# Kernel optimization log

Hardware: AMD Instinct MI355X
Metric: run time of the kernel (lower is better)

## Reference

```python
import jax, jax.numpy as jnp
import numpy as np

B, C, H, W = 8, 512, 64, 64
CH = C // 2          # channels per branch after chunk
R = CH // 4          # reduced channels (reduction=4)


def conv1x1(x, w, b):
    # x: [B,c,H,W], w: [o,c], b: [o]  (1x1 conv == per-pixel matmul)
    return jnp.einsum('oc,bchw->bohw', w, x) + b[None, :, None, None]


def spatial_self_corr(x, w1, b1, w2, b2, wo, bo):
    # DANet-style position attention. x: [B,CH,H,W]
    b_, c_, h_, w_ = x.shape
    n = h_ * w_
    q = conv1x1(x, w1, b1).reshape(b_, -1, n)   # [B,R,N]
    k = conv1x1(x, w2, b2).reshape(b_, -1, n)   # [B,R,N]
    attn = jax.nn.softmax(jnp.einsum('brn,brm->bnm', q, k), axis=-1)  # [B,N,N]
    out = jnp.einsum('brn,bnm->brm', k, attn)   # v = k (reduced channels), [B,R,N]
    out = out.reshape(b_, -1, h_, w_)
    return conv1x1(out, wo, bo)                 # [B,CH,H,W]


def channel_self_corr(x, wq, bq, wk, bk, wo, bo):
    # DANet-style channel attention over reduced channels. x: [B,CH,H,W]
    b_, c_, h_, w_ = x.shape
    n = h_ * w_
    q = conv1x1(x, wq, bq).reshape(b_, -1, n)   # [B,R,N]
    k = conv1x1(x, wk, bk).reshape(b_, -1, n)   # [B,R,N]
    attn = jax.nn.softmax(jnp.einsum('brn,bsn->brs', q, k), axis=-1)  # [B,R,R]
    out = jnp.einsum('brs,bsn->brn', attn, k)   # v = k (reduced channels)
    out = out.reshape(b_, -1, h_, w_)
    return conv1x1(out, wo, bo)                 # [B,CH,H,W]


def ckam_forward(top_feat, bottom_feat, wt, bt, wb, bb,
                 s_w1, s_b1, s_w2, s_b2, s_wo, s_bo,
                 c_wq, c_bq, c_wk, c_bk, c_wo, c_bo, f_w, f_b):
    top = conv1x1(top_feat, wt, bt)
    bottom = conv1x1(bottom_feat, wb, bb)
    x = top + bottom                            # [B,C,H,W]
    x1, x2 = jnp.split(x, 2, axis=1)            # each [B,C/2,H,W]
    ssc_out = spatial_self_corr(x1, s_w1, s_b1, s_w2, s_b2, s_wo, s_bo)
    csc_out = channel_self_corr(x2, c_wq, c_bq, c_wk, c_bk, c_wo, c_bo)
    out = jnp.concatenate([ssc_out, csc_out], axis=1)  # [B,C,H,W]
    return conv1x1(out, f_w, f_b)


def setup_inputs() -> dict:
    key = jax.random.key(0)
    ks = jax.random.split(key, 24)
    s = 0.02
    d = {
        'top_feat': jax.random.normal(ks[0], (B, C, H, W), jnp.float32),
        'bottom_feat': jax.random.normal(ks[1], (B, C, H, W), jnp.float32),
        'wt': jax.random.normal(ks[2], (C, C), jnp.float32) * s,
        'bt': jnp.zeros((C,), jnp.float32),
        'wb': jax.random.normal(ks[3], (C, C), jnp.float32) * s,
        'bb': jnp.zeros((C,), jnp.float32),
        's_w1': jax.random.normal(ks[4], (R, CH), jnp.float32) * s,
        's_b1': jnp.zeros((R,), jnp.float32),
        's_w2': jax.random.normal(ks[5], (R, CH), jnp.float32) * s,
        's_b2': jnp.zeros((R,), jnp.float32),
        's_wo': jax.random.normal(ks[6], (CH, R), jnp.float32) * s,
        's_bo': jnp.zeros((CH,), jnp.float32),
        'c_wq': jax.random.normal(ks[7], (R, CH), jnp.float32) * s,
        'c_bq': jnp.zeros((R,), jnp.float32),
        'c_wk': jax.random.normal(ks[8], (R, CH), jnp.float32) * s,
        'c_bk': jnp.zeros((R,), jnp.float32),
        'c_wo': jax.random.normal(ks[9], (CH, R), jnp.float32) * s,
        'c_bo': jnp.zeros((CH,), jnp.float32),
        'f_w': jax.random.normal(ks[10], (C, C), jnp.float32) * s,
        'f_b': jnp.zeros((C,), jnp.float32),
    }
    return d


def reference(top_feat, bottom_feat, wt, bt, wb, bb,
              s_w1, s_b1, s_w2, s_b2, s_wo, s_bo,
              c_wq, c_bq, c_wk, c_bk, c_wo, c_bo, f_w, f_b):
    return ckam_forward(top_feat, bottom_feat, wt, bt, wb, bb,
                        s_w1, s_b1, s_w2, s_b2, s_wo, s_bo,
                        c_wq, c_bq, c_wk, c_bk, c_wo, c_bo, f_w, f_b)
```

## Files before the change

### kernel.cpp

```cpp
#include <hip/hip_runtime.h>

typedef unsigned short u16;
typedef unsigned int   u32;
typedef __attribute__((ext_vector_type(8))) short short8;
typedef __attribute__((ext_vector_type(4))) float f32x4;

__device__ __forceinline__ u16 f2bf(float f) {
  u32 u = __float_as_uint(f);
  u32 r = u + 0x7fffu + ((u >> 16) & 1u);
  return (u16)(r >> 16);
}

__device__ __forceinline__ void gl_lds16(const u16* g, u16* l) {
  __builtin_amdgcn_global_load_lds(
      (const __attribute__((address_space(1))) u32*)g,
      (__attribute__((address_space(3))) u32*)l, 16, 0, 0);
}

__global__ __launch_bounds__(256) void k_combine_qk(
    const float* __restrict__ wt, const float* __restrict__ bt,
    const float* __restrict__ wb, const float* __restrict__ bb,
    const float* __restrict__ s_w1, const float* __restrict__ s_b1,
    const float* __restrict__ s_w2, const float* __restrict__ s_b2,
    const float* __restrict__ c_wq, const float* __restrict__ c_bq,
    const float* __restrict__ c_wk, const float* __restrict__ c_bk,
    u16* __restrict__ Wqkb, float* __restrict__ bqk) {
  int j = blockIdx.x;
  int g = j >> 6, r = j & 63;
  const float* sw; const float* sb;
  if (g == 0)      { sw = s_w1; sb = s_b1; }
  else if (g == 1) { sw = s_w2; sb = s_b2; }
  else if (g == 2) { sw = c_wq; sb = c_bq; }
  else             { sw = c_wk; sb = c_bk; }
  int cbase = (g < 2) ? 0 : 256;

  __shared__ float swr[256];
  __shared__ float red[256];
  int t = threadIdx.x;
  swr[t] = sw[r * 256 + t];
  __syncthreads();

  float a0 = 0.f, a1 = 0.f, a2 = 0.f, a3 = 0.f;
#pragma unroll 4
  for (int c = 0; c < 256; ++c) {
    float a = swr[c];
    int row = (cbase + c) * 512;
    a0 += a * wt[row + t];
    a1 += a * wt[row + 256 + t];
    a2 += a * wb[row + t];
    a3 += a * wb[row + 256 + t];
  }
  Wqkb[j * 1024 + t]       = f2bf(a0);
  Wqkb[j * 1024 + 256 + t] = f2bf(a1);
  Wqkb[j * 1024 + 512 + t] = f2bf(a2);
  Wqkb[j * 1024 + 768 + t] = f2bf(a3);

  red[t] = swr[t] * (bt[cbase + t] + bb[cbase + t]);
  __syncthreads();
  for (int s = 128; s > 0; s >>= 1) {
    if (t < s) red[t] += red[t + s];
    __syncthreads();
  }
  if (t == 0) bqk[j] = red[0] + sb[r];
}

__global__ __launch_bounds__(128) void k_combine_f(
    const float* __restrict__ f_w, const float* __restrict__ f_b,
    const float* __restrict__ s_wo, const float* __restrict__ s_bo,
    const float* __restrict__ c_wo, const float* __restrict__ c_bo,
    u16* __restrict__ Wfb, float* __restrict__ bfb) {
  int o = blockIdx.x;
  int t = threadIdx.x;
  __shared__ float fwr[512];
  __shared__ float red[128];
  for (int i = t; i < 512; i += 128) fwr[i] = f_w[o * 512 + i];
  __syncthreads();

  float acc = 0.f;
  if (t < 64) {
#pragma unroll 4
    for (int c = 0; c < 256; ++c) acc += fwr[c] * s_wo[c * 64 + t];
  } else {
    int rr = t - 64;
#pragma unroll 4
    for (int c = 0; c < 256; ++c) acc += fwr[256 + c] * c_wo[c * 64 + rr];
  }
  Wfb[o * 128 + t] = f2bf(acc);

  red[t] = fwr[t] * s_bo[t] + fwr[t + 128] * s_bo[t + 128]
         + fwr[256 + t] * c_bo[t] + fwr[384 + t] * c_bo[t + 128];
  __syncthreads();
  for (int s = 64; s > 0; s >>= 1) {
    if (t < s) red[t] += red[t + s];
    __syncthreads();
  }
  if (t == 0) bfb[o] = red[0] + f_b[o];
}

__global__ __launch_bounds__(256) void k_gemm_qk_mfma(
    const float* __restrict__ top, const float* __restrict__ bot,
    const u16* __restrict__ Wqkb, const float* __restrict__ bqk,
    float* __restrict__ qk) {
  int b = blockIdx.z, j0 = blockIdx.y * 128, n0 = blockIdx.x * 128;
  __shared__ __align__(16) u16 Aj[2][128][32];
  __shared__ __align__(16) u16 Xs[2][128][32];
  int t = threadIdx.x;
  int wv = t >> 6, lane = t & 63;
  int wr = wv >> 1, wc = wv & 1;
  int q = lane >> 4, l = lane & 15;

  f32x4 acc[4][4];
#pragma unroll
  for (int tr = 0; tr < 4; ++tr)
#pragma unroll
    for (int tc = 0; tc < 4; ++tc) acc[tr][tc] = (f32x4){0.f, 0.f, 0.f, 0.f};

  int xn = t & 31;
  int xs = t >> 5;
  int asrow = (lane >> 2);
  int asc = (lane & 3) ^ ((lane >> 2) & 3);
  int fsw = (q ^ (l & 3)) << 4;

  float xv[16];

  auto stageA = [&](int kc, u16* dst) {
#pragma unroll
    for (int p = 0; p < 2; ++p) {
      int cI = wv * 2 + p;
      int row = cI * 16 + asrow;
      gl_lds16(Wqkb + (size_t)(j0 + row) * 1024 + kc + asc * 8, dst + cI * 512);
    }
  };
  auto loadX = [&](int kc) {
    const float* src = (kc < 512) ? top : bot;
    int c0 = kc & 511;
    const float* xb = src + (size_t)(b * 512 + c0) * 4096 + n0;
#pragma unroll
    for (int p = 0; p < 8; ++p) {
      int n = xn + 32 * (p >> 1);
      int kp = xs + 8 * (p & 1);
      xv[2 * p]     = xb[(size_t)(2 * kp) * 4096 + n];
      xv[2 * p + 1] = xb[(size_t)(2 * kp + 1) * 4096 + n];
    }
  };
  auto writeX = [&](u16* dst) {
    char* base = reinterpret_cast<char*>(dst);
#pragma unroll
    for (int p = 0; p < 8; ++p) {
      int n = xn + 32 * (p >> 1);
      int kp = xs + 8 * (p & 1);
      u32 v = (u32)f2bf(xv[2 * p]) | ((u32)f2bf(xv[2 * p + 1]) << 16);
      *reinterpret_cast<u32*>(
          base + n * 64 + ((((kp >> 2) ^ (n & 3)) << 4) | ((kp & 3) << 2))) = v;
    }
  };

  stageA(0, &Aj[0][0][0]);
  loadX(0);
  writeX(&Xs[0][0][0]);
  __syncthreads();

  int cur = 0;
  for (int it = 0; it < 32; ++it) {
    if (it + 1 < 32) {
      stageA((it + 1) * 32, &Aj[cur ^ 1][0][0]);
      loadX((it + 1) * 32);
    }
    const char* Ab = reinterpret_cast<const char*>(&Aj[cur][0][0]);
    const char* Xb = reinterpret_cast<const char*>(&Xs[cur][0][0]);
    short8 af[4], bfr[4];
#pragma unroll
    for (int tr = 0; tr < 4; ++tr) {
      int row = wr * 64 + tr * 16 + l;
      af[tr] = *reinterpret_cast<const short8*>(Ab + row * 64 + fsw);
    }
#pragma unroll
    for (int tc = 0; tc < 4; ++tc) {
      int row = wc * 64 + tc * 16 + l;
      bfr[tc] = *reinterpret_cast<const short8*>(Xb + row * 64 + fsw);
    }
#pragma unroll
    for (int tr = 0; tr < 4; ++tr)
#pragma unroll
      for (int tc = 0; tc < 4; ++tc)
        acc[tr][tc] = __builtin_amdgcn_mfma_f32_16x16x32_bf16(
            af[tr], bfr[tc], acc[tr][tc], 0, 0, 0);
    if (it + 1 < 32) writeX(&Xs[cur ^ 1][0][0]);
    __syncthreads();
    cur ^= 1;
  }

#pragma unroll
  for (int tr = 0; tr < 4; ++tr) {
    int j = j0 + wr * 64 + tr * 16 + q * 4;
    float4 bias = *reinterpret_cast<const float4*>(&bqk[j]);
#pragma unroll
    for (int tc = 0; tc < 4; ++tc) {
      int n = n0 + wc * 64 + tc * 16 + l;
      float* dst = qk + (size_t)(b * 256 + j) * 4096 + n;
      dst[0]        = acc[tr][tc][0] + bias.x;
      dst[4096]     = acc[tr][tc][1] + bias.y;
      dst[2 * 4096] = acc[tr][tc][2] + bias.z;
      dst[3 * 4096] = acc[tr][tc][3] + bias.w;
    }
  }
}

__global__ __launch_bounds__(256) void k_transpose_qk(
    const float* __restrict__ qk, u16* __restrict__ q1t, u16* __restrict__ k1t) {
  int b = blockIdx.y, n0 = blockIdx.x * 64;
  __shared__ u16 T[128][68];
  int t = threadIdx.x;
  for (int i = t; i < 8192; i += 256) {
    int j = i >> 6, n = i & 63;
    T[j][n] = f2bf(qk[((size_t)(b * 256) + j) * 4096 + n0 + n]);
  }
  __syncthreads();
  int n = t & 63, h = t >> 6;
  u16 buf[32];
#pragma unroll
  for (int jj = 0; jj < 32; ++jj) buf[jj] = T[h * 32 + jj][n];
  u16* dst;
  if (h < 2) dst = q1t + ((size_t)(b * 4096) + n0 + n) * 64 + h * 32;
  else       dst = k1t + ((size_t)(b * 4096) + n0 + n) * 64 + (h - 2) * 32;
  u32* d32 = reinterpret_cast<u32*>(dst);
#pragma unroll
  for (int k = 0; k < 16; ++k)
    d32[k] = (u32)buf[2 * k] | ((u32)buf[2 * k + 1] << 16);
}

__global__ __launch_bounds__(256) void k_sp_stats_mfma(
    const u16* __restrict__ q1t, const u16* __restrict__ k1t,
    float* __restrict__ dinv) {
  int b = blockIdx.y, n0 = blockIdx.x * 64;
  __shared__ u16 Qs[64][72];
  __shared__ float red[4][64][16];
  int t = threadIdx.x;
  int wv = t >> 6, lane = t & 63;
  int q = lane >> 4, l = lane & 15;

  {
    const u32* src = reinterpret_cast<const u32*>(q1t + ((size_t)(b * 4096) + n0) * 64);
    for (int i = t; i < 2048; i += 256) {
      int n = i >> 5, c = i & 31;
      reinterpret_cast<u32*>(&Qs[n][0])[c] = src[n * 32 + c];
    }
  }
  __syncthreads();

  short8 afr[4][2];
#pragma unroll
  for (int tn = 0; tn < 4; ++tn)
#pragma unroll
    for (int kh = 0; kh < 2; ++kh)
      afr[tn][kh] = *reinterpret_cast<const short8*>(&Qs[tn * 16 + l][kh * 32 + q * 8]);

  const u16* kbase = k1t + (size_t)b * 4096 * 64;
  float dsum[4][4];
#pragma unroll
  for (int tn = 0; tn < 4; ++tn)
#pragma unroll
    for (int i = 0; i < 4; ++i) dsum[tn][i] = 0.f;

  for (int mt = wv; mt < 64; mt += 4) {
    int m0 = mt * 64;
#pragma unroll
    for (int tm = 0; tm < 4; ++tm) {
      const u16* kp = kbase + ((size_t)(m0 + tm * 16 + l)) * 64;
      short8 b0 = *reinterpret_cast<const short8*>(kp + q * 8);
      short8 b1 = *reinterpret_cast<const short8*>(kp + 32 + q * 8);
#pragma unroll
      for (int tn = 0; tn < 4; ++tn) {
        f32x4 acc = {0.f, 0.f, 0.f, 0.f};
        acc = __builtin_amdgcn_mfma_f32_16x16x32_bf16(afr[tn][0], b0, acc, 0, 0, 0);
        acc = __builtin_amdgcn_mfma_f32_16x16x32_bf16(afr[tn][1], b1, acc, 0, 0, 0);
#pragma unroll
        for (int i = 0; i < 4; ++i) dsum[tn][i] += __expf(acc[i]);
      }
    }
  }

#pragma unroll
  for (int tn = 0; tn < 4; ++tn)
#pragma unroll
    for (int i = 0; i < 4; ++i)
      red[wv][tn * 16 + q * 4 + i][l] = dsum[tn][i];
  __syncthreads();
  if (t < 64) {
    float s = 0.f;
#pragma unroll
    for (int v = 0; v < 4; ++v)
#pragma unroll
      for (int u = 0; u < 16; ++u) s += red[v][t][u];
    dinv[(size_t)b * 4096 + n0 + t] = 1.0f / s;
  }
}

__global__ __launch_bounds__(256) void k_scale_k1d(
    const float* __restrict__ qk, const float* __restrict__ dinv,
    u16* __restrict__ k1d) {
  int b = blockIdx.x >> 6, r = blockIdx.x & 63;
  const float* src = qk + ((size_t)(b * 256) + 64 + r) * 4096;
  const float* dv = dinv + (size_t)b * 4096;
  u16* dst = k1d + ((size_t)(b * 64) + r) * 4096;
  for (int i = threadIdx.x; i < 4096; i += 256)
    dst[i] = f2bf(src[i] * dv[i]);
}

#define NSPLIT 2

__device__ __forceinline__ void stage_qk(const u16* qb, const u16* kb, int noff,
                                         u16* qdst, u16* kdst,
                                         int wv, int rsub, int scol) {
#pragma unroll
  for (int pp = 0; pp < 2; ++pp) {
    int p = wv * 2 + pp;
    int row = p * 8 + rsub;
    gl_lds16(qb + ((size_t)(noff + row)) * 64 + scol * 8, qdst + p * 512);
    gl_lds16(kb + (size_t)row * 4096 + noff + scol * 8, kdst + p * 512);
  }
}

__global__ __launch_bounds__(256) void k_sp_apply_mfma(
    const u16* __restrict__ q1t, const u16* __restrict__ k1t,
    const u16* __restrict__ k1d, float* __restrict__ spre) {
  int b = blockIdx.z, m0 = blockIdx.x * 64;
  int n_base = blockIdx.y * (4096 / NSPLIT);
  const int NT = 64 / NSPLIT;

  __shared__ __align__(16) u16 Qs[2][64][64];
  __shared__ __align__(16) u16 Ks[2][64][64];
  __shared__ __align__(16) u16 Wt[64][64];

  int t = threadIdx.x;
  int wv = t >> 6, lane = t & 63;
  int q = lane >> 4, l = lane & 15;
  int sw = l & 7;
  int rsub = lane >> 3;
  int scol = (lane & 7) ^ rsub;

  const u16* ktp = k1t + ((size_t)(b * 4096) + m0 + wv * 16 + l) * 64;
  short8 bS0 = *reinterpret_cast<const short8*>(ktp + q * 8);
  short8 bS1 = *reinterpret_cast<const short8*>(ktp + 32 + q * 8);

  const u16* qb = q1t + (size_t)b * 4096 * 64;
  const u16* kb = k1d + (size_t)b * 64 * 4096;

  f32x4 accO[4];
#pragma unroll
  for (int tr = 0; tr < 4; ++tr) accO[tr] = (f32x4){0.f, 0.f, 0.f, 0.f};

  stage_qk(qb, kb, n_base, &Qs[0][0][0], &Ks[0][0][0], wv, rsub, scol);
  __syncthreads();

  int wrow = wv * 16 + l;
  char* wp = reinterpret_cast<char*>(&Wt[wrow][0]);
  int c_a0 = (q ^ sw) << 4;
  int c_a1 = c_a0 ^ 64;

  int cur = 0;
  for (int nt = 0; nt < NT; ++nt) {
    if (nt + 1 < NT)
      stage_qk(qb, kb, n_base + (nt + 1) * 64,
               &Qs[cur ^ 1][0][0], &Ks[cur ^ 1][0][0], wv, rsub, scol);

    const u16(*Qc)[64] = Qs[cur];
    const u16(*Kc)[64] = Ks[cur];

#pragma unroll
    for (int tn = 0; tn < 4; ++tn) {
      const char* qrow = reinterpret_cast<const char*>(&Qc[tn * 16 + l][0]);
      short8 a0 = *reinterpret_cast<const short8*>(qrow + c_a0);
      short8 a1 = *reinterpret_cast<const short8*>(qrow + c_a1);
      f32x4 s = {0.f, 0.f, 0.f, 0.f};
      s = __builtin_amdgcn_mfma_f32_16x16x32_bf16(a0, bS0, s, 0, 0, 0);
      s = __builtin_amdgcn_mfma_f32_16x16x32_bf16(a1, bS1, s, 0, 0, 0);
      u16 w0 = f2bf(__expf(s[0]));
      u16 w1 = f2bf(__expf(s[1]));
      u16 w2 = f2bf(__expf(s[2]));
      u16 w3 = f2bf(__expf(s[3]));
      uint2 pk;
      pk.x = (u32)w0 | ((u32)w1 << 16);
      pk.y = (u32)w2 | ((u32)w3 << 16);
      *reinterpret_cast<uint2*>(
          wp + ((((tn * 2 + (q >> 1)) ^ sw) << 4) | ((q & 1) << 3))) = pk;
    }

    short8 bW0 = *reinterpret_cast<const short8*>(wp + c_a0);
    short8 bW1 = *reinterpret_cast<const short8*>(wp + c_a1);
#pragma unroll
    for (int tr = 0; tr < 4; ++tr) {
      const char* krow = reinterpret_cast<const char*>(&Kc[tr * 16 + l][0]);
      short8 a0 = *reinterpret_cast<const short8*>(krow + c_a0);
      short8 a1 = *reinterpret_cast<const short8*>(krow + c_a1);
      accO[tr] = __builtin_amdgcn_mfma_f32_16x16x32_bf16(a0, bW0, accO[tr], 0, 0, 0);
      accO[tr] = __builtin_amdgcn_mfma_f32_16x16x32_bf16(a1, bW1, accO[tr], 0, 0, 0);
    }

    __syncthreads();
    cur ^= 1;
  }

#pragma unroll
  for (int tr = 0; tr < 4; ++tr)
#pragma unroll
    for (int i = 0; i < 4; ++i)
      atomicAdd(&spre[(size_t)(b * 64 + tr * 16 + q * 4 + i) * 4096 + m0 + wrow],
                accO[tr][i]);
}

__global__ __launch_bounds__(256) void k_ch_scores(
    const float* __restrict__ qk, float* __restrict__ part) {
  int b = blockIdx.y, ch = blockIdx.x;
  const float* q2 = qk + (size_t)(b * 256 + 128) * 4096;
  const float* k2 = qk + (size_t)(b * 256 + 192) * 4096;
  __shared__ float Qs[64][65];
  __shared__ float Ks[64][65];
  int t = threadIdx.x, ti = t >> 4, tj = t & 15;
  float acc[4][4] = {};

  for (int sub = 0; sub < 2; ++sub) {
    int n0 = ch * 128 + sub * 64;
    __syncthreads();
    for (int i = t; i < 4096; i += 256) {
      int r = i >> 6, n = i & 63;
      Qs[r][n] = q2[(size_t)r * 4096 + n0 + n];
      Ks[r][n] = k2[(size_t)r * 4096 + n0 + n];
    }
    __syncthreads();
#pragma unroll
    for (int n = 0; n < 64; ++n) {
      float qa[4], ka[4];
#pragma unroll
      for (int i = 0; i < 4; ++i) qa[i] = Qs[ti * 4 + i][n];
#pragma unroll
      for (int jx = 0; jx < 4; ++jx) ka[jx] = Ks[tj * 4 + jx][n];
#pragma unroll
      for (int i = 0; i < 4; ++i)
#pragma unroll
        for (int jx = 0; jx < 4; ++jx) acc[i][jx] += qa[i] * ka[jx];
    }
  }
#pragma unroll
  for (int i = 0; i < 4; ++i)
#pragma unroll
    for (int jx = 0; jx < 4; ++jx)
      part[(size_t)(b * 32 + ch) * 4096 + (ti * 4 + i) * 64 + tj * 4 + jx] = acc[i][jx];
}

__global__ __launch_bounds__(64) void k_ch_softmax(
    const float* __restrict__ part, float* __restrict__ attn2) {
  int bid = blockIdx.x;
  int b = bid >> 6, r = bid & 63;
  int s = threadIdx.x;
  const float* p0 = part + (size_t)(b * 32) * 4096 + r * 64 + s;
  float sum = 0.f;
#pragma unroll
  for (int c = 0; c < 32; ++c) sum += p0[(size_t)c * 4096];
  float mx = sum;
#pragma unroll
  for (int o = 32; o > 0; o >>= 1) mx = fmaxf(mx, __shfl_xor(mx, o));
  float e = __expf(sum - mx);
  float den = e;
#pragma unroll
  for (int o = 32; o > 0; o >>= 1) den += __shfl_xor(den, o);
  attn2[(size_t)b * 4096 + r * 64 + s] = e / den;
}

__global__ __launch_bounds__(256) void k_ch_apply(
    const float* __restrict__ qk, const float* __restrict__ attn2,
    float* __restrict__ cpre) {
  int b = blockIdx.y;
  int t = threadIdx.x;
  int n = blockIdx.x * 64 + (t & 63);
  int qr = t >> 6;
  const float* k2 = qk + (size_t)(b * 256 + 192) * 4096;
  __shared__ float As[64][64];
  {
    float4* As4 = reinterpret_cast<float4*>(&As[0][0]);
    const float4* a4 = reinterpret_cast<const float4*>(attn2 + (size_t)b * 4096);
    for (int i = t; i < 1024; i += 256) As4[i] = a4[i];
  }
  __syncthreads();

  float acc[16];
#pragma unroll
  for (int rr = 0; rr < 16; ++rr) acc[rr] = 0.f;
  for (int s4 = 0; s4 < 64; s4 += 4) {
    float kv0 = k2[(size_t)(s4 + 0) * 4096 + n];
    float kv1 = k2[(size_t)(s4 + 1) * 4096 + n];
    float kv2 = k2[(size_t)(s4 + 2) * 4096 + n];
    float kv3 = k2[(size_t)(s4 + 3) * 4096 + n];
#pragma unroll
    for (int rr = 0; rr < 16; ++rr) {
      float4 w = *reinterpret_cast<const float4*>(&As[qr * 16 + rr][s4]);
      acc[rr] += w.x * kv0 + w.y * kv1 + w.z * kv2 + w.w * kv3;
    }
  }
#pragma unroll
  for (int rr = 0; rr < 16; ++rr)
    cpre[(size_t)(b * 64 + qr * 16 + rr) * 4096 + n] = acc[rr];
}

__global__ __launch_bounds__(256) void k_final_mfma(
    const float* __restrict__ spre, const float* __restrict__ cpre,
    const u16* __restrict__ Wfb, const float* __restrict__ bfb,
    float* __restrict__ out) {
  int b = blockIdx.z, o0 = blockIdx.y * 128, n0 = blockIdx.x * 128;
  __shared__ u16 Aj[128][40];
  __shared__ u16 Xs[128][40];
  int t = threadIdx.x;
  int wv = t >> 6, lane = t & 63;
  int wr = wv >> 1, wc = wv & 1;
  int q = lane >> 4, l = lane & 15;

  f32x4 acc[4][4];
#pragma unroll
  for (int tr = 0; tr < 4; ++tr)
#pragma unroll
    for (int tc = 0; tc < 4; ++tc) acc[tr][tc] = (f32x4){0.f, 0.f, 0.f, 0.f};

  int xn = t & 31;
  int xs = t >> 5;

  for (int kc = 0; kc < 128; kc += 32) {
    __syncthreads();
    {
      const u32* asrc = reinterpret_cast<const u32*>(Wfb + (size_t)o0 * 128 + kc);
#pragma unroll
      for (int p = 0; p < 8; ++p) {
        int i = p * 256 + t;
        int row = i >> 4, c = i & 15;
        *reinterpret_cast<u32*>(&Aj[row][c * 2]) = asrc[(size_t)row * 64 + c];
      }
    }
    const float* src = (kc < 64) ? spre : cpre;
    int r0 = (kc < 64) ? kc : kc - 64;
    const float* xb = src + (size_t)(b * 64 + r0) * 4096 + n0;
#pragma unroll
    for (int p = 0; p < 8; ++p) {
      int n = xn + 32 * (p >> 1);
      int kp = xs + 8 * (p & 1);
      float v0 = xb[(size_t)(2 * kp) * 4096 + n];
      float v1 = xb[(size_t)(2 * kp + 1) * 4096 + n];
      *reinterpret_cast<u32*>(&Xs[n][kp * 2]) =
          (u32)f2bf(v0) | ((u32)f2bf(v1) << 16);
    }
    __syncthreads();

    short8 af[4], bfr[4];
#pragma unroll
    for (int tr = 0; tr < 4; ++tr)
      af[tr] = *reinterpret_cast<const short8*>(&Aj[wr * 64 + tr * 16 + l][q * 8]);
#pragma unroll
    for (int tc = 0; tc < 4; ++tc)
      bfr[tc] = *reinterpret_cast<const short8*>(&Xs[wc * 64 + tc * 16 + l][q * 8]);
#pragma unroll
    for (int tr = 0; tr < 4; ++tr)
#pragma unroll
      for (int tc = 0; tc < 4; ++tc)
        acc[tr][tc] = __builtin_amdgcn_mfma_f32_16x16x32_bf16(
            af[tr], bfr[tc], acc[tr][tc], 0, 0, 0);
  }

#pragma unroll
  for (int tr = 0; tr < 4; ++tr) {
    int o = o0 + wr * 64 + tr * 16 + q * 4;
    float4 bias = *reinterpret_cast<const float4*>(&bfb[o]);
#pragma unroll
    for (int tc = 0; tc < 4; ++tc) {
      int n = n0 + wc * 64 + tc * 16 + l;
      float* dst = out + (size_t)(b * 512 + o) * 4096 + n;
      dst[0]        = acc[tr][tc][0] + bias.x;
      dst[4096]     = acc[tr][tc][1] + bias.y;
      dst[2 * 4096] = acc[tr][tc][2] + bias.z;
      dst[3 * 4096] = acc[tr][tc][3] + bias.w;
    }
  }
}

extern "C" void kernel_launch(void* const* d_in, const int* in_sizes, int n_in,
                              void* d_out, int out_size, void* d_ws, size_t ws_size,
                              hipStream_t stream) {
  const float* top  = (const float*)d_in[0];
  const float* bot  = (const float*)d_in[1];
  const float* wt   = (const float*)d_in[2];
  const float* bt   = (const float*)d_in[3];
  const float* wb   = (const float*)d_in[4];
  const float* bb   = (const float*)d_in[5];
  const float* s_w1 = (const float*)d_in[6];
  const float* s_b1 = (const float*)d_in[7];
  const float* s_w2 = (const float*)d_in[8];
  const float* s_b2 = (const float*)d_in[9];
  const float* s_wo = (const float*)d_in[10];
  const float* s_bo = (const float*)d_in[11];
  const float* c_wq = (const float*)d_in[12];
  const float* c_bq = (const float*)d_in[13];
  const float* c_wk = (const float*)d_in[14];
  const float* c_bk = (const float*)d_in[15];
  const float* c_wo = (const float*)d_in[16];
  const float* c_bo = (const float*)d_in[17];
  const float* f_w  = (const float*)d_in[18];
  const float* f_b  = (const float*)d_in[19];
  float* out = (float*)d_out;

  char* ob = (char*)d_out;
  float* qk = (float*)ob;
  u16* q1t = (u16*)(ob + 33554432);
  u16* k1t = (u16*)(ob + 37748736);
  u16* k1d = (u16*)(ob + 41943040);
  float* part = (float*)(ob + 46137344);

  char* ws = (char*)d_ws;
  float* dinv  = (float*)(ws + 0);
  float* attn2 = (float*)(ws + 1179648);
  float* spre  = (float*)(ws + 1310720);
  float* cpre  = (float*)(ws + 9699328);
  u16*   Wqkb  = (u16*)  (ws + 18087936);
  float* bqk   = (float*)(ws + 18612224);
  u16*   Wfb   = (u16*)  (ws + 18613248);
  float* bfb   = (float*)(ws + 18744320);

  hipMemsetAsync(spre, 0, 8388608, stream);

  k_combine_qk<<<256, 256, 0, stream>>>(wt, bt, wb, bb, s_w1, s_b1, s_w2, s_b2,
                                        c_wq, c_bq, c_wk, c_bk, Wqkb, bqk);
  k_combine_f<<<512, 128, 0, stream>>>(f_w, f_b, s_wo, s_bo, c_wo, c_bo, Wfb, bfb);
  k_gemm_qk_mfma<<<dim3(32, 2, 8), 256, 0, stream>>>(top, bot, Wqkb, bqk, qk);
  k_transpose_qk<<<dim3(64, 8), 256, 0, stream>>>(qk, q1t, k1t);
  k_sp_stats_mfma<<<dim3(64, 8), 256, 0, stream>>>(q1t, k1t, dinv);
  k_ch_scores<<<dim3(32, 8), 256, 0, stream>>>(qk, part);
  k_ch_softmax<<<512, 64, 0, stream>>>(part, attn2);
  k_ch_apply<<<dim3(64, 8), 256, 0, stream>>>(qk, attn2, cpre);
  k_scale_k1d<<<512, 256, 0, stream>>>(qk, dinv, k1d);
  k_sp_apply_mfma<<<dim3(64, NSPLIT, 8), 256, 0, stream>>>(q1t, k1t, k1d, spre);
  k_final_mfma<<<dim3(32, 4, 8), 256, 0, stream>>>(spre, cpre, Wfb, bfb, out);
}
```

Measured before the change: 447.9 us.

## Deepen X prefetch to two stages and repack LDS writes with new swizzle

The QK projection GEMM now holds two register buffers of X so global loads run two k-steps ahead of compute, with a manually unrolled ping-pong loop. Each thread now loads four consecutive channels per pixel and writes 8-byte packed bf16 values to LDS instead of 4-byte ones. The LDS swizzle is changed on both the staging and fragment-read sides to suit the new write pattern. The extra register buffer raises VGPR pressure, which could reduce occupancy.

```diff
diff --git a/kernel.cpp b/kernel.cpp
--- a/kernel.cpp
+++ b/kernel.cpp
@@ -117,78 +117,90 @@
 
   int xn = t & 31;
   int xs = t >> 5;
-  int asrow = (lane >> 2);
-  int asc = (lane & 3) ^ ((lane >> 2) & 3);
-  int fsw = (q ^ (l & 3)) << 4;
-
-  float xv[16];
+  int kx = (xn + (xn >> 2)) & 3;
+  int wcol = ((((xs >> 1) ^ kx) << 4) | ((xs & 1) << 3));
+  int asr4 = lane >> 2;
+  int asc = (lane & 3) ^ ((asr4 + (asr4 >> 2)) & 3);
+  int rowA = wr * 64 + l;
+  int rowX = wc * 64 + l;
+  int fswA = (q ^ ((rowA + (rowA >> 2)) & 3)) << 4;
+  int fswX = (q ^ ((rowX + (rowX >> 2)) & 3)) << 4;
+
+  float xva[16], xvb[16];
 
   auto stageA = [&](int kc, u16* dst) {
 #pragma unroll
-    for (int p = 0; p < 2; ++p) {
-      int cI = wv * 2 + p;
-      int row = cI * 16 + asrow;
-      gl_lds16(Wqkb + (size_t)(j0 + row) * 1024 + kc + asc * 8, dst + cI * 512);
+    for (int pp = 0; pp < 2; ++pp) {
+      int p = wv * 2 + pp;
+      int row = p * 16 + asr4;
+      gl_lds16(Wqkb + (size_t)(j0 + row) * 1024 + kc + asc * 8, dst + p * 512);
     }
   };
-  auto loadX = [&](int kc) {
+  auto loadX = [&](int kc, float (&xv)[16]) {
     const float* src = (kc < 512) ? top : bot;
     int c0 = kc & 511;
     const float* xb = src + (size_t)(b * 512 + c0) * 4096 + n0;
 #pragma unroll
-    for (int p = 0; p < 8; ++p) {
-      int n = xn + 32 * (p >> 1);
-      int kp = xs + 8 * (p & 1);
-      xv[2 * p]     = xb[(size_t)(2 * kp) * 4096 + n];
-      xv[2 * p + 1] = xb[(size_t)(2 * kp + 1) * 4096 + n];
+    for (int p = 0; p < 4; ++p) {
+      int n = xn + 32 * p;
+#pragma unroll
+      for (int d = 0; d < 4; ++d)
+        xv[4 * p + d] = xb[(size_t)(4 * xs + d) * 4096 + n];
     }
   };
-  auto writeX = [&](u16* dst) {
+  auto writeX = [&](float (&xv)[16], u16* dst) {
     char* base = reinterpret_cast<char*>(dst);
 #pragma unroll
-    for (int p = 0; p < 8; ++p) {
-      int n = xn + 32 * (p >> 1);
-      int kp = xs + 8 * (p & 1);
-      u32 v = (u32)f2bf(xv[2 * p]) | ((u32)f2bf(xv[2 * p + 1]) << 16);
-      *reinterpret_cast<u32*>(
-          base + n * 64 + ((((kp >> 2) ^ (n & 3)) << 4) | ((kp & 3) << 2))) = v;
+    for (int p = 0; p < 4; ++p) {
+      int n = xn + 32 * p;
+      uint2 pk;
+      pk.x = (u32)f2bf(xv[4 * p])     | ((u32)f2bf(xv[4 * p + 1]) << 16);
+      pk.y = (u32)f2bf(xv[4 * p + 2]) | ((u32)f2bf(xv[4 * p + 3]) << 16);
+      *reinterpret_cast<uint2*>(base + n * 64 + wcol) = pk;
     }
   };
-
-  stageA(0, &Aj[0][0][0]);
-  loadX(0);
-  writeX(&Xs[0][0][0]);
-  __syncthreads();
-
-  int cur = 0;
-  for (int it = 0; it < 32; ++it) {
-    if (it + 1 < 32) {
-      stageA((it + 1) * 32, &Aj[cur ^ 1][0][0]);
-      loadX((it + 1) * 32);
-    }
-    const char* Ab = reinterpret_cast<const char*>(&Aj[cur][0][0]);
-    const char* Xb = reinterpret_cast<const char*>(&Xs[cur][0][0]);
+  auto compute = [&](int bufsel) {
+    const char* Ab = reinterpret_cast<const char*>(&Aj[bufsel][0][0]);
+    const char* Xb = reinterpret_cast<const char*>(&Xs[bufsel][0][0]);
     short8 af[4], bfr[4];
 #pragma unroll
-    for (int tr = 0; tr < 4; ++tr) {
-      int row = wr * 64 + tr * 16 + l;
-      af[tr] = *reinterpret_cast<const short8*>(Ab + row * 64 + fsw);
-    }
-#pragma unroll
-    for (int tc = 0; tc < 4; ++tc) {
-      int row = wc * 64 + tc * 16 + l;
-      bfr[tc] = *reinterpret_cast<const short8*>(Xb + row * 64 + fsw);
-    }
+    for (int tr = 0; tr < 4; ++tr)
+      af[tr] = *reinterpret_cast<const short8*>(Ab + (rowA + tr * 16) * 64 + fswA);
+#pragma unroll
+    for (int tc = 0; tc < 4; ++tc)
+      bfr[tc] = *reinterpret_cast<const short8*>(Xb + (rowX + tc * 16) * 64 + fswX);
 #pragma unroll
     for (int tr = 0; tr < 4; ++tr)
 #pragma unroll
       for (int tc = 0; tc < 4; ++tc)
         acc[tr][tc] = __builtin_amdgcn_mfma_f32_16x16x32_bf16(
             af[tr], bfr[tc], acc[tr][tc], 0, 0, 0);
-    if (it + 1 < 32) writeX(&Xs[cur ^ 1][0][0]);
-    __syncthreads();
-    cur ^= 1;
-  }
+  };
+
+  loadX(0, xva);
+  stageA(0, &Aj[0][0][0]);
+  writeX(xva, &Xs[0][0][0]);
+  loadX(32, xvb);
+  __syncthreads();
+
+  for (int it2 = 0; it2 < 15; ++it2) {
+    int e = it2 * 2;
+    loadX((e + 2) * 32, xva);
+    stageA((e + 1) * 32, &Aj[1][0][0]);
+    writeX(xvb, &Xs[1][0][0]);
+    compute(0);
+    __syncthreads();
+    loadX((e + 3) * 32, xvb);
+    stageA((e + 2) * 32, &Aj[0][0][0]);
+    writeX(xva, &Xs[0][0][0]);
+    compute(1);
+    __syncthreads();
+  }
+  stageA(31 * 32, &Aj[1][0][0]);
+  writeX(xvb, &Xs[1][0][0]);
+  compute(0);
+  __syncthreads();
+  compute(1);
 
 #pragma unroll
   for (int tr = 0; tr < 4; ++tr) {
```

Result: faster. 436.4 us (-2.6%).
